# Performance work log

Measured on AMD Instinct MI355X. Metric: run time of the kernel, lower is better.

Reference implementation:

```python
import jax, jax.numpy as jnp
import numpy as np

ATT_TIMES = 2
EPS = 1e-12  # torch F.normalize eps

N_NODES = 200000
EMB_DIM = 256
ATT_NUM = 2


def setup_inputs() -> dict:
    key = jax.random.key(0)
    k1, k2 = jax.random.split(key)
    x = jax.random.normal(k1, (N_NODES, EMB_DIM), dtype=jnp.float32)
    # glorot/xavier-normal init for the att_num projection matrices W_i
    std = float(np.sqrt(2.0 / (EMB_DIM + EMB_DIM)))
    W = jax.random.normal(k2, (ATT_NUM, EMB_DIM, EMB_DIM), dtype=jnp.float32) * std
    return {"x": x, "W": W}


def _one_attention(x, Wi):
    """One attention head (att_style='dot', att_weight=True), iterated ATT_TIMES."""
    xi = x
    out = None
    for _ in range(ATT_TIMES):
        temp = jnp.mean(xi, axis=0, keepdims=True)          # (1, D)
        h_avg = jnp.tanh(temp @ Wi)                          # (1, D)
        # 'dot' style: interact with W = identity -> scores = x @ h_avg^T, (N, 1)
        scores = xi @ h_avg.T                                # (N, 1)
        # F.normalize(p=1, dim=1) on an (N,1) column: divide by max(|v|, eps)
        norm = jnp.maximum(jnp.sum(jnp.abs(scores), axis=1, keepdims=True), EPS)
        att = jax.nn.sigmoid(scores / norm)                  # (N, 1)
        out = att.T @ xi                                     # (1, D)
        xi = xi * att                                        # re-weight for next round
    return out


def reference(x, W):
    att_num = W.shape[0]
    outs = [_one_attention(x, W[i]) for i in range(att_num)]
    return jnp.concatenate(outs, axis=1)                     # (1, att_num * D)
```

## Files before the change

### kernel.cpp

```cpp
#include <hip/hip_runtime.h>
#include <math.h>

#define NROWS 200000
#define D 256
#define F4 64

#define NBLK 500
#define CHUNK 400
#define ITERS 25

#define WS_H1 0
#define WS_H2 512
#define WS_A  1024
#define WS_P1 401024
#define WS_P2 529024

__device__ __forceinline__ float att_sigmoid(float s) {
    float t = s / fmaxf(fabsf(s), 1e-12f);
    return 1.0f / (1.0f + __expf(-t));
}

__device__ __forceinline__ float wave_sum(float v) {
#pragma unroll
    for (int off = 1; off < 64; off <<= 1) v += __shfl_xor(v, off);
    return v;
}

__device__ __forceinline__ float dot4(float4 a, float4 b) {
    return fmaf(a.x, b.x, fmaf(a.y, b.y, fmaf(a.z, b.z, a.w * b.w)));
}

__global__ void __launch_bounds__(256) colsum_kernel(const float* __restrict__ x,
                                                     float* __restrict__ part) {
    const int tid = threadIdx.x, lane = tid & 63, wv = tid >> 6;
    const float4* x4 = reinterpret_cast<const float4*>(x);
    const size_t base = (size_t)(blockIdx.x * CHUNK + wv * 4) * F4 + lane;
    float4 cur[4], nxt[4];
#pragma unroll
    for (int j = 0; j < 4; ++j) cur[j] = x4[base + j * F4];
    float4 accA = make_float4(0.f, 0.f, 0.f, 0.f);
    float4 accB = make_float4(0.f, 0.f, 0.f, 0.f);
    for (int it = 0; it < ITERS; ++it) {
        if (it + 1 < ITERS) {
            size_t nb = base + (size_t)(it + 1) * 16 * F4;
#pragma unroll
            for (int j = 0; j < 4; ++j) nxt[j] = x4[nb + j * F4];
        }
        accA.x += cur[0].x + cur[1].x; accB.x += cur[2].x + cur[3].x;
        accA.y += cur[0].y + cur[1].y; accB.y += cur[2].y + cur[3].y;
        accA.z += cur[0].z + cur[1].z; accB.z += cur[2].z + cur[3].z;
        accA.w += cur[0].w + cur[1].w; accB.w += cur[2].w + cur[3].w;
        if (it + 1 < ITERS) {
#pragma unroll
            for (int j = 0; j < 4; ++j) cur[j] = nxt[j];
        }
    }
    accA.x += accB.x; accA.y += accB.y; accA.z += accB.z; accA.w += accB.w;
    __shared__ float4 sh[256];
    sh[tid] = accA;
    __syncthreads();
    if (tid < 64) {
        float4 a = sh[tid], b = sh[tid + 64], c = sh[tid + 128], d = sh[tid + 192];
        float4 s;
        s.x = (a.x + b.x) + (c.x + d.x);
        s.y = (a.y + b.y) + (c.y + d.y);
        s.z = (a.z + b.z) + (c.z + d.z);
        s.w = (a.w + b.w) + (c.w + d.w);
        reinterpret_cast<float4*>(part + blockIdx.x * 256)[tid] = s;
    }
}

__global__ void __launch_bounds__(256) hproj_fused(const float* __restrict__ W,
                                                   const float* __restrict__ part,
                                                   int width, int headColMul, float scale,
                                                   float* __restrict__ hout) {
    const int head = blockIdx.x;
    const int tid = threadIdx.x, lane = tid & 63, wv = tid >> 6;
    const float* p = part + head * headColMul + lane * 4;
    float4 s = make_float4(0.f, 0.f, 0.f, 0.f);
    for (int i = 0; i < 25; ++i) {
        float4 v[5];
#pragma unroll
        for (int k = 0; k < 5; ++k)
            v[k] = *reinterpret_cast<const float4*>(p + (size_t)(wv + (i * 5 + k) * 4) * width);
#pragma unroll
        for (int k = 0; k < 5; ++k) {
            s.x += v[k].x; s.y += v[k].y; s.z += v[k].z; s.w += v[k].w;
        }
    }
    __shared__ float4 red[4][64];
    __shared__ float vbuf[D];
    red[wv][lane] = s;
    __syncthreads();
    if (tid < 64) {
        float4 a = red[0][tid], b = red[1][tid], c = red[2][tid], d = red[3][tid];
        vbuf[tid * 4 + 0] = ((a.x + b.x) + (c.x + d.x)) * scale;
        vbuf[tid * 4 + 1] = ((a.y + b.y) + (c.y + d.y)) * scale;
        vbuf[tid * 4 + 2] = ((a.z + b.z) + (c.z + d.z)) * scale;
        vbuf[tid * 4 + 3] = ((a.w + b.w) + (c.w + d.w)) * scale;
    }
    __syncthreads();
    const float* Wh = W + head * D * D;
    float acc = 0.0f;
#pragma unroll 8
    for (int k = 0; k < D; ++k) acc = fmaf(vbuf[k], Wh[k * D + tid], acc);
    hout[head * D + tid] = tanhf(acc);
}

__global__ void __launch_bounds__(256) pass1_kernel(const float* __restrict__ x,
                                                    float* __restrict__ ws) {
    const float* h = ws + WS_H1;
    float* aA0 = ws + WS_A;
    float* aA1 = ws + WS_A + NROWS;
    float* part = ws + WS_P2;
    const int tid = threadIdx.x, lane = tid & 63, wv = tid >> 6;
    const int r0 = blockIdx.x * CHUNK + wv * 4;
    const float4* x4 = reinterpret_cast<const float4*>(x);
    const float4 h0v = reinterpret_cast<const float4*>(h)[lane];
    const float4 h1v = reinterpret_cast<const float4*>(h + D)[lane];
    float4 acc0 = make_float4(0.f, 0.f, 0.f, 0.f);
    float4 acc1 = make_float4(0.f, 0.f, 0.f, 0.f);
    const size_t base = (size_t)r0 * F4 + lane;
    float4 cur[4], nxt[4];
#pragma unroll
    for (int j = 0; j < 4; ++j) cur[j] = x4[base + j * F4];
    for (int it = 0; it < ITERS; ++it) {
        if (it + 1 < ITERS) {
            size_t nb = base + (size_t)(it + 1) * 16 * F4;
#pragma unroll
            for (int j = 0; j < 4; ++j) nxt[j] = x4[nb + j * F4];
        }
        float d0[4], d1[4];
#pragma unroll
        for (int j = 0; j < 4; ++j) { d0[j] = dot4(cur[j], h0v); d1[j] = dot4(cur[j], h1v); }
#pragma unroll
        for (int j = 0; j < 4; ++j) { d0[j] = wave_sum(d0[j]); d1[j] = wave_sum(d1[j]); }
        float a0[4], a1[4];
#pragma unroll
        for (int j = 0; j < 4; ++j) {
            a0[j] = att_sigmoid(d0[j]);
            a1[j] = att_sigmoid(d1[j]);
            acc0.x = fmaf(a0[j], cur[j].x, acc0.x);
            acc0.y = fmaf(a0[j], cur[j].y, acc0.y);
            acc0.z = fmaf(a0[j], cur[j].z, acc0.z);
            acc0.w = fmaf(a0[j], cur[j].w, acc0.w);
            acc1.x = fmaf(a1[j], cur[j].x, acc1.x);
            acc1.y = fmaf(a1[j], cur[j].y, acc1.y);
            acc1.z = fmaf(a1[j], cur[j].z, acc1.z);
            acc1.w = fmaf(a1[j], cur[j].w, acc1.w);
        }
        const int rb = r0 + it * 16;
        if (lane == 0)
            *reinterpret_cast<float4*>(aA0 + rb) = make_float4(a0[0], a0[1], a0[2], a0[3]);
        else if (lane == 1)
            *reinterpret_cast<float4*>(aA1 + rb) = make_float4(a1[0], a1[1], a1[2], a1[3]);
        if (it + 1 < ITERS) {
#pragma unroll
            for (int j = 0; j < 4; ++j) cur[j] = nxt[j];
        }
    }
    __shared__ float4 sh[2][256];
    sh[0][tid] = acc0;
    sh[1][tid] = acc1;
    __syncthreads();
    if (tid < 128) {
        int hh = tid >> 6;
        int t = tid & 63;
        float4 a = sh[hh][t], b = sh[hh][t + 64], c = sh[hh][t + 128], d = sh[hh][t + 192];
        float4 s;
        s.x = (a.x + b.x) + (c.x + d.x);
        s.y = (a.y + b.y) + (c.y + d.y);
        s.z = (a.z + b.z) + (c.z + d.z);
        s.w = (a.w + b.w) + (c.w + d.w);
        reinterpret_cast<float4*>(part + blockIdx.x * 512)[tid] = s;
    }
}

__global__ void __launch_bounds__(256) pass2_kernel(const float* __restrict__ x,
                                                    float* __restrict__ ws) {
    const float* h = ws + WS_H2;
    const float* aA0 = ws + WS_A;
    const float* aA1 = ws + WS_A + NROWS;
    float* part = ws + WS_P2;
    const int tid = threadIdx.x, lane = tid & 63, wv = tid >> 6;
    const int r0 = blockIdx.x * CHUNK + wv * 4;
    const float4* x4 = reinterpret_cast<const float4*>(x);
    const float4 h0v = reinterpret_cast<const float4*>(h)[lane];
    const float4 h1v = reinterpret_cast<const float4*>(h + D)[lane];
    float4 acc0 = make_float4(0.f, 0.f, 0.f, 0.f);
    float4 acc1 = make_float4(0.f, 0.f, 0.f, 0.f);
    const size_t base = (size_t)r0 * F4 + lane;
    float4 cur[4], nxt[4];
    float4 caa0, caa1, naa0, naa1;
#pragma unroll
    for (int j = 0; j < 4; ++j) cur[j] = x4[base + j * F4];
    caa0 = *reinterpret_cast<const float4*>(aA0 + r0);
    caa1 = *reinterpret_cast<const float4*>(aA1 + r0);
    for (int it = 0; it < ITERS; ++it) {
        if (it + 1 < ITERS) {
            size_t nb = base + (size_t)(it + 1) * 16 * F4;
#pragma unroll
            for (int j = 0; j < 4; ++j) nxt[j] = x4[nb + j * F4];
            naa0 = *reinterpret_cast<const float4*>(aA0 + r0 + (it + 1) * 16);
            naa1 = *reinterpret_cast<const float4*>(aA1 + r0 + (it + 1) * 16);
        }
        float d0[4], d1[4];
#pragma unroll
        for (int j = 0; j < 4; ++j) { d0[j] = dot4(cur[j], h0v); d1[j] = dot4(cur[j], h1v); }
#pragma unroll
        for (int j = 0; j < 4; ++j) { d0[j] = wave_sum(d0[j]); d1[j] = wave_sum(d1[j]); }
        float w0[4], w1[4];
        w0[0] = att_sigmoid(caa0.x * d0[0]) * caa0.x;
        w0[1] = att_sigmoid(caa0.y * d0[1]) * caa0.y;
        w0[2] = att_sigmoid(caa0.z * d0[2]) * caa0.z;
        w0[3] = att_sigmoid(caa0.w * d0[3]) * caa0.w;
        w1[0] = att_sigmoid(caa1.x * d1[0]) * caa1.x;
        w1[1] = att_sigmoid(caa1.y * d1[1]) * caa1.y;
        w1[2] = att_sigmoid(caa1.z * d1[2]) * caa1.z;
        w1[3] = att_sigmoid(caa1.w * d1[3]) * caa1.w;
#pragma unroll
        for (int j = 0; j < 4; ++j) {
            acc0.x = fmaf(w0[j], cur[j].x, acc0.x);
            acc0.y = fmaf(w0[j], cur[j].y, acc0.y);
            acc0.z = fmaf(w0[j], cur[j].z, acc0.z);
            acc0.w = fmaf(w0[j], cur[j].w, acc0.w);
            acc1.x = fmaf(w1[j], cur[j].x, acc1.x);
            acc1.y = fmaf(w1[j], cur[j].y, acc1.y);
            acc1.z = fmaf(w1[j], cur[j].z, acc1.z);
            acc1.w = fmaf(w1[j], cur[j].w, acc1.w);
        }
        if (it + 1 < ITERS) {
#pragma unroll
            for (int j = 0; j < 4; ++j) cur[j] = nxt[j];
            caa0 = naa0; caa1 = naa1;
        }
    }
    __shared__ float4 sh[2][256];
    sh[0][tid] = acc0;
    sh[1][tid] = acc1;
    __syncthreads();
    if (tid < 128) {
        int hh = tid >> 6;
        int t = tid & 63;
        float4 a = sh[hh][t], b = sh[hh][t + 64], c = sh[hh][t + 128], d = sh[hh][t + 192];
        float4 s;
        s.x = (a.x + b.x) + (c.x + d.x);
        s.y = (a.y + b.y) + (c.y + d.y);
        s.z = (a.z + b.z) + (c.z + d.z);
        s.w = (a.w + b.w) + (c.w + d.w);
        reinterpret_cast<float4*>(part + blockIdx.x * 512)[tid] = s;
    }
}

__global__ void __launch_bounds__(256) out_reduce(const float* __restrict__ part,
                                                  float* __restrict__ out) {
    const int head = blockIdx.x;
    const int tid = threadIdx.x, lane = tid & 63, wv = tid >> 6;
    const float* p = part + head * 256 + lane * 4;
    float4 s = make_float4(0.f, 0.f, 0.f, 0.f);
    for (int i = 0; i < 25; ++i) {
        float4 v[5];
#pragma unroll
        for (int k = 0; k < 5; ++k)
            v[k] = *reinterpret_cast<const float4*>(p + (size_t)(wv + (i * 5 + k) * 4) * 512);
#pragma unroll
        for (int k = 0; k < 5; ++k) {
            s.x += v[k].x; s.y += v[k].y; s.z += v[k].z; s.w += v[k].w;
        }
    }
    __shared__ float4 red[4][64];
    red[wv][lane] = s;
    __syncthreads();
    if (tid < 64) {
        float4 a = red[0][tid], b = red[1][tid], c = red[2][tid], d = red[3][tid];
        float4 o;
        o.x = (a.x + b.x) + (c.x + d.x);
        o.y = (a.y + b.y) + (c.y + d.y);
        o.z = (a.z + b.z) + (c.z + d.z);
        o.w = (a.w + b.w) + (c.w + d.w);
        reinterpret_cast<float4*>(out + head * 256)[tid] = o;
    }
}

extern "C" void kernel_launch(void* const* d_in, const int* in_sizes, int n_in,
                              void* d_out, int out_size, void* d_ws, size_t ws_size,
                              hipStream_t stream) {
    const float* x = (const float*)d_in[0];
    const float* W = (const float*)d_in[1];
    float* out = (float*)d_out;
    float* ws = (float*)d_ws;

    colsum_kernel<<<dim3(NBLK), dim3(256), 0, stream>>>(x, ws + WS_P1);
    hproj_fused<<<dim3(2), dim3(256), 0, stream>>>(W, ws + WS_P1, 256, 0, 1.0f / NROWS, ws + WS_H1);
    pass1_kernel<<<dim3(NBLK), dim3(256), 0, stream>>>(x, ws);
    hproj_fused<<<dim3(2), dim3(256), 0, stream>>>(W, ws + WS_P2, 512, 256, 1.0f / NROWS, ws + WS_H2);
    pass2_kernel<<<dim3(NBLK), dim3(256), 0, stream>>>(x, ws);
    out_reduce<<<dim3(2), dim3(256), 0, stream>>>(ws + WS_P2, out);
}
```

Before: 167.2 us.

## Map one row per 16-lane group and raise block count for streaming passes

```diff
diff --git a/kernel.cpp b/kernel.cpp
--- a/kernel.cpp
+++ b/kernel.cpp
@@ -5,29 +5,29 @@
 #define D 256
 #define F4 64
 
-#define NBLK 500
-#define CHUNK 400
-#define ITERS 25
+#define NBLK 1250
+#define CHUNK 160
+#define ITERS 10
 
 #define WS_H1 0
 #define WS_H2 512
 #define WS_A  1024
 #define WS_P1 401024
-#define WS_P2 529024
+#define WS_P2 721024
 
 __device__ __forceinline__ float att_sigmoid(float s) {
     float t = s / fmaxf(fabsf(s), 1e-12f);
     return 1.0f / (1.0f + __expf(-t));
 }
 
-__device__ __forceinline__ float wave_sum(float v) {
-#pragma unroll
-    for (int off = 1; off < 64; off <<= 1) v += __shfl_xor(v, off);
-    return v;
-}
-
 __device__ __forceinline__ float dot4(float4 a, float4 b) {
     return fmaf(a.x, b.x, fmaf(a.y, b.y, fmaf(a.z, b.z, a.w * b.w)));
+}
+
+__device__ __forceinline__ float group16_sum(float v) {
+#pragma unroll
+    for (int off = 1; off < 16; off <<= 1) v += __shfl_xor(v, off);
+    return v;
 }
 
 __global__ void __launch_bounds__(256) colsum_kernel(const float* __restrict__ x,
@@ -66,27 +66,22 @@
         s.y = (a.y + b.y) + (c.y + d.y);
         s.z = (a.z + b.z) + (c.z + d.z);
         s.w = (a.w + b.w) + (c.w + d.w);
-        reinterpret_cast<float4*>(part + blockIdx.x * 256)[tid] = s;
+        reinterpret_cast<float4*>(part)[blockIdx.x * 64 + tid] = s;
     }
 }
 
 __global__ void __launch_bounds__(256) hproj_fused(const float* __restrict__ W,
                                                    const float* __restrict__ part,
-                                                   int width, int headColMul, float scale,
+                                                   int width4, int headOff4, float scale,
                                                    float* __restrict__ hout) {
     const int head = blockIdx.x;
     const int tid = threadIdx.x, lane = tid & 63, wv = tid >> 6;
-    const float* p = part + head * headColMul + lane * 4;
+    const float4* p4 = reinterpret_cast<const float4*>(part) + head * headOff4 + lane;
     float4 s = make_float4(0.f, 0.f, 0.f, 0.f);
-    for (int i = 0; i < 25; ++i) {
-        float4 v[5];
-#pragma unroll
-        for (int k = 0; k < 5; ++k)
-            v[k] = *reinterpret_cast<const float4*>(p + (size_t)(wv + (i * 5 + k) * 4) * width);
-#pragma unroll
-        for (int k = 0; k < 5; ++k) {
-            s.x += v[k].x; s.y += v[k].y; s.z += v[k].z; s.w += v[k].w;
-        }
+#pragma unroll 5
+    for (int r = wv; r < NBLK; r += 4) {
+        float4 v = p4[(size_t)r * width4];
+        s.x += v.x; s.y += v.y; s.z += v.z; s.w += v.w;
     }
     __shared__ float4 red[4][64];
     __shared__ float vbuf[D];
@@ -114,65 +109,70 @@
     float* aA1 = ws + WS_A + NROWS;
     float* part = ws + WS_P2;
     const int tid = threadIdx.x, lane = tid & 63, wv = tid >> 6;
-    const int r0 = blockIdx.x * CHUNK + wv * 4;
+    const int sub = lane >> 4, li = lane & 15;
     const float4* x4 = reinterpret_cast<const float4*>(x);
-    const float4 h0v = reinterpret_cast<const float4*>(h)[lane];
-    const float4 h1v = reinterpret_cast<const float4*>(h + D)[lane];
-    float4 acc0 = make_float4(0.f, 0.f, 0.f, 0.f);
-    float4 acc1 = make_float4(0.f, 0.f, 0.f, 0.f);
-    const size_t base = (size_t)r0 * F4 + lane;
+    const float4* h4 = reinterpret_cast<const float4*>(h);
+    float4 h0v[4], h1v[4];
+#pragma unroll
+    for (int t = 0; t < 4; ++t) { h0v[t] = h4[li + 16 * t]; h1v[t] = h4[64 + li + 16 * t]; }
+    const int row0 = blockIdx.x * CHUNK + wv * 4 + sub;
+    const size_t base = (size_t)row0 * F4 + li;
     float4 cur[4], nxt[4];
 #pragma unroll
-    for (int j = 0; j < 4; ++j) cur[j] = x4[base + j * F4];
+    for (int t = 0; t < 4; ++t) cur[t] = x4[base + 16 * t];
+    float4 acc0[4], acc1[4];
+#pragma unroll
+    for (int t = 0; t < 4; ++t) {
+        acc0[t] = make_float4(0.f, 0.f, 0.f, 0.f);
+        acc1[t] = make_float4(0.f, 0.f, 0.f, 0.f);
+    }
     for (int it = 0; it < ITERS; ++it) {
         if (it + 1 < ITERS) {
             size_t nb = base + (size_t)(it + 1) * 16 * F4;
 #pragma unroll
-            for (int j = 0; j < 4; ++j) nxt[j] = x4[nb + j * F4];
-        }
-        float d0[4], d1[4];
-#pragma unroll
-        for (int j = 0; j < 4; ++j) { d0[j] = dot4(cur[j], h0v); d1[j] = dot4(cur[j], h1v); }
-#pragma unroll
-        for (int j = 0; j < 4; ++j) { d0[j] = wave_sum(d0[j]); d1[j] = wave_sum(d1[j]); }
-        float a0[4], a1[4];
-#pragma unroll
-        for (int j = 0; j < 4; ++j) {
-            a0[j] = att_sigmoid(d0[j]);
-            a1[j] = att_sigmoid(d1[j]);
-            acc0.x = fmaf(a0[j], cur[j].x, acc0.x);
-            acc0.y = fmaf(a0[j], cur[j].y, acc0.y);
-            acc0.z = fmaf(a0[j], cur[j].z, acc0.z);
-            acc0.w = fmaf(a0[j], cur[j].w, acc0.w);
-            acc1.x = fmaf(a1[j], cur[j].x, acc1.x);
-            acc1.y = fmaf(a1[j], cur[j].y, acc1.y);
-            acc1.z = fmaf(a1[j], cur[j].z, acc1.z);
-            acc1.w = fmaf(a1[j], cur[j].w, acc1.w);
-        }
-        const int rb = r0 + it * 16;
-        if (lane == 0)
-            *reinterpret_cast<float4*>(aA0 + rb) = make_float4(a0[0], a0[1], a0[2], a0[3]);
-        else if (lane == 1)
-            *reinterpret_cast<float4*>(aA1 + rb) = make_float4(a1[0], a1[1], a1[2], a1[3]);
-        if (it + 1 < ITERS) {
-#pragma unroll
-            for (int j = 0; j < 4; ++j) cur[j] = nxt[j];
-        }
-    }
-    __shared__ float4 sh[2][256];
-    sh[0][tid] = acc0;
-    sh[1][tid] = acc1;
+            for (int t = 0; t < 4; ++t) nxt[t] = x4[nb + 16 * t];
+        }
+        float d0 = (dot4(cur[0], h0v[0]) + dot4(cur[1], h0v[1]))
+                 + (dot4(cur[2], h0v[2]) + dot4(cur[3], h0v[3]));
+        float d1 = (dot4(cur[0], h1v[0]) + dot4(cur[1], h1v[1]))
+                 + (dot4(cur[2], h1v[2]) + dot4(cur[3], h1v[3]));
+        d0 = group16_sum(d0);
+        d1 = group16_sum(d1);
+        float a0 = att_sigmoid(d0);
+        float a1 = att_sigmoid(d1);
+        if (li == 0) {
+            aA0[row0 + it * 16] = a0;
+            aA1[row0 + it * 16] = a1;
+        }
+#pragma unroll
+        for (int t = 0; t < 4; ++t) {
+            acc0[t].x = fmaf(a0, cur[t].x, acc0[t].x);
+            acc0[t].y = fmaf(a0, cur[t].y, acc0[t].y);
+            acc0[t].z = fmaf(a0, cur[t].z, acc0[t].z);
+            acc0[t].w = fmaf(a0, cur[t].w, acc0[t].w);
+            acc1[t].x = fmaf(a1, cur[t].x, acc1[t].x);
+            acc1[t].y = fmaf(a1, cur[t].y, acc1[t].y);
+            acc1[t].z = fmaf(a1, cur[t].z, acc1[t].z);
+            acc1[t].w = fmaf(a1, cur[t].w, acc1[t].w);
+        }
+        if (it + 1 < ITERS) {
+#pragma unroll
+            for (int t = 0; t < 4; ++t) cur[t] = nxt[t];
+        }
+    }
+    __shared__ float4 sh[256][9];
+#pragma unroll
+    for (int t = 0; t < 4; ++t) { sh[tid][t] = acc0[t]; sh[tid][4 + t] = acc1[t]; }
     __syncthreads();
     if (tid < 128) {
-        int hh = tid >> 6;
-        int t = tid & 63;
-        float4 a = sh[hh][t], b = sh[hh][t + 64], c = sh[hh][t + 128], d = sh[hh][t + 192];
-        float4 s;
-        s.x = (a.x + b.x) + (c.x + d.x);
-        s.y = (a.y + b.y) + (c.y + d.y);
-        s.z = (a.z + b.z) + (c.z + d.z);
-        s.w = (a.w + b.w) + (c.w + d.w);
-        reinterpret_cast<float4*>(part + blockIdx.x * 512)[tid] = s;
+        const int hh = tid >> 6, f = tid & 63, fl = f & 15, ft = f >> 4;
+        float4 s = make_float4(0.f, 0.f, 0.f, 0.f);
+#pragma unroll
+        for (int g = 0; g < 16; ++g) {
+            float4 v = sh[(g >> 2) * 64 + (g & 3) * 16 + fl][hh * 4 + ft];
+            s.x += v.x; s.y += v.y; s.z += v.z; s.w += v.w;
+        }
+        reinterpret_cast<float4*>(part)[blockIdx.x * 128 + tid] = s;
     }
 }
 
@@ -183,72 +183,72 @@
     const float* aA1 = ws + WS_A + NROWS;
     float* part = ws + WS_P2;
     const int tid = threadIdx.x, lane = tid & 63, wv = tid >> 6;
-    const int r0 = blockIdx.x * CHUNK + wv * 4;
+    const int sub = lane >> 4, li = lane & 15;
     const float4* x4 = reinterpret_cast<const float4*>(x);
-    const float4 h0v = reinterpret_cast<const float4*>(h)[lane];
-    const float4 h1v = reinterpret_cast<const float4*>(h + D)[lane];
-    float4 acc0 = make_float4(0.f, 0.f, 0.f, 0.f);
-    float4 acc1 = make_float4(0.f, 0.f, 0.f, 0.f);
-    const size_t base = (size_t)r0 * F4 + lane;
+    const float4* h4 = reinterpret_cast<const float4*>(h);
+    float4 h0v[4], h1v[4];
+#pragma unroll
+    for (int t = 0; t < 4; ++t) { h0v[t] = h4[li + 16 * t]; h1v[t] = h4[64 + li + 16 * t]; }
+    const int row0 = blockIdx.x * CHUNK + wv * 4 + sub;
+    const size_t base = (size_t)row0 * F4 + li;
     float4 cur[4], nxt[4];
-    float4 caa0, caa1, naa0, naa1;
-#pragma unroll
-    for (int j = 0; j < 4; ++j) cur[j] = x4[base + j * F4];
-    caa0 = *reinterpret_cast<const float4*>(aA0 + r0);
-    caa1 = *reinterpret_cast<const float4*>(aA1 + r0);
+    float caa0, caa1, naa0, naa1;
+#pragma unroll
+    for (int t = 0; t < 4; ++t) cur[t] = x4[base + 16 * t];
+    caa0 = aA0[row0];
+    caa1 = aA1[row0];
+    float4 acc0[4], acc1[4];
+#pragma unroll
+    for (int t = 0; t < 4; ++t) {
+        acc0[t] = make_float4(0.f, 0.f, 0.f, 0.f);
+        acc1[t] = make_float4(0.f, 0.f, 0.f, 0.f);
+    }
     for (int it = 0; it < ITERS; ++it) {
         if (it + 1 < ITERS) {
             size_t nb = base + (size_t)(it + 1) * 16 * F4;
 #pragma unroll
-            for (int j = 0; j < 4; ++j) nxt[j] = x4[nb + j * F4];
-            naa0 = *reinterpret_cast<const float4*>(aA0 + r0 + (it + 1) * 16);
-            naa1 = *reinterpret_cast<const float4*>(aA1 + r0 + (it + 1) * 16);
-        }
-        float d0[4], d1[4];
-#pragma unroll
-        for (int j = 0; j < 4; ++j) { d0[j] = dot4(cur[j], h0v); d1[j] = dot4(cur[j], h1v); }
-#pragma unroll
-        for (int j = 0; j < 4; ++j) { d0[j] = wave_sum(d0[j]); d1[j] = wave_sum(d1[j]); }
-        float w0[4], w1[4];
-        w0[0] = att_sigmoid(caa0.x * d0[0]) * caa0.x;
-        w0[1] = att_sigmoid(caa0.y * d0[1]) * caa0.y;
-        w0[2] = att_sigmoid(caa0.z * d0[2]) * caa0.z;
-        w0[3] = att_sigmoid(caa0.w * d0[3]) * caa0.w;
-        w1[0] = att_sigmoid(caa1.x * d1[0]) * caa1.x;
-        w1[1] = att_sigmoid(caa1.y * d1[1]) * caa1.y;
-        w1[2] = att_sigmoid(caa1.z * d1[2]) * caa1.z;
-        w1[3] = att_sigmoid(caa1.w * d1[3]) * caa1.w;
-#pragma unroll
-        for (int j = 0; j < 4; ++j) {
-            acc0.x = fmaf(w0[j], cur[j].x, acc0.x);
-            acc0.y = fmaf(w0[j], cur[j].y, acc0.y);
-            acc0.z = fmaf(w0[j], cur[j].z, acc0.z);
-            acc0.w = fmaf(w0[j], cur[j].w, acc0.w);
-            acc1.x = fmaf(w1[j], cur[j].x, acc1.x);
-            acc1.y = fmaf(w1[j], cur[j].y, acc1.y);
-            acc1.z = fmaf(w1[j], cur[j].z, acc1.z);
-            acc1.w = fmaf(w1[j], cur[j].w, acc1.w);
-        }
-        if (it + 1 < ITERS) {
-#pragma unroll
-            for (int j = 0; j < 4; ++j) cur[j] = nxt[j];
+            for (int t = 0; t < 4; ++t) nxt[t] = x4[nb + 16 * t];
+            naa0 = aA0[row0 + (it + 1) * 16];
+            naa1 = aA1[row0 + (it + 1) * 16];
+        }
+        float d0 = (dot4(cur[0], h0v[0]) + dot4(cur[1], h0v[1]))
+                 + (dot4(cur[2], h0v[2]) + dot4(cur[3], h0v[3]));
+        float d1 = (dot4(cur[0], h1v[0]) + dot4(cur[1], h1v[1]))
+                 + (dot4(cur[2], h1v[2]) + dot4(cur[3], h1v[3]));
+        d0 = group16_sum(d0);
+        d1 = group16_sum(d1);
+        float w0 = att_sigmoid(caa0 * d0) * caa0;
+        float w1 = att_sigmoid(caa1 * d1) * caa1;
+#pragma unroll
+        for (int t = 0; t < 4; ++t) {
+            acc0[t].x = fmaf(w0, cur[t].x, acc0[t].x);
+            acc0[t].y = fmaf(w0, cur[t].y, acc0[t].y);
+            acc0[t].z = fmaf(w0, cur[t].z, acc0[t].z);
+            acc0[t].w = fmaf(w0, cur[t].w, acc0[t].w);
+            acc1[t].x = fmaf(w1, cur[t].x, acc1[t].x);
+            acc1[t].y = fmaf(w1, cur[t].y, acc1[t].y);
+            acc1[t].z = fmaf(w1, cur[t].z, acc1[t].z);
+            acc1[t].w = fmaf(w1, cur[t].w, acc1[t].w);
+        }
+        if (it + 1 < ITERS) {
+#pragma unroll
+            for (int t = 0; t < 4; ++t) cur[t] = nxt[t];
             caa0 = naa0; caa1 = naa1;
         }
     }
-    __shared__ float4 sh[2][256];
-    sh[0][tid] = acc0;
-    sh[1][tid] = acc1;
+    __shared__ float4 sh[256][9];
+#pragma unroll
+    for (int t = 0; t < 4; ++t) { sh[tid][t] = acc0[t]; sh[tid][4 + t] = acc1[t]; }
     __syncthreads();
     if (tid < 128) {
-        int hh = tid >> 6;
-        int t = tid & 63;
-        float4 a = sh[hh][t], b = sh[hh][t + 64], c = sh[hh][t + 128], d = sh[hh][t + 192];
-        float4 s;
-        s.x = (a.x + b.x) + (c.x + d.x);
-        s.y = (a.y + b.y) + (c.y + d.y);
-        s.z = (a.z + b.z) + (c.z + d.z);
-        s.w = (a.w + b.w) + (c.w + d.w);
-        reinterpret_cast<float4*>(part + blockIdx.x * 512)[tid] = s;
+        const int hh = tid >> 6, f = tid & 63, fl = f & 15, ft = f >> 4;
+        float4 s = make_float4(0.f, 0.f, 0.f, 0.f);
+#pragma unroll
+        for (int g = 0; g < 16; ++g) {
+            float4 v = sh[(g >> 2) * 64 + (g & 3) * 16 + fl][hh * 4 + ft];
+            s.x += v.x; s.y += v.y; s.z += v.z; s.w += v.w;
+        }
+        reinterpret_cast<float4*>(part)[blockIdx.x * 128 + tid] = s;
     }
 }
 
@@ -256,17 +256,12 @@
                                                   float* __restrict__ out) {
     const int head = blockIdx.x;
     const int tid = threadIdx.x, lane = tid & 63, wv = tid >> 6;
-    const float* p = part + head * 256 + lane * 4;
+    const float4* p4 = reinterpret_cast<const float4*>(part) + head * 64 + lane;
     float4 s = make_float4(0.f, 0.f, 0.f, 0.f);
-    for (int i = 0; i < 25; ++i) {
-        float4 v[5];
-#pragma unroll
-        for (int k = 0; k < 5; ++k)
-            v[k] = *reinterpret_cast<const float4*>(p + (size_t)(wv + (i * 5 + k) * 4) * 512);
-#pragma unroll
-        for (int k = 0; k < 5; ++k) {
-            s.x += v[k].x; s.y += v[k].y; s.z += v[k].z; s.w += v[k].w;
-        }
+#pragma unroll 5
+    for (int r = wv; r < NBLK; r += 4) {
+        float4 v = p4[(size_t)r * 128];
+        s.x += v.x; s.y += v.y; s.z += v.z; s.w += v.w;
     }
     __shared__ float4 red[4][64];
     red[wv][lane] = s;
@@ -278,7 +273,7 @@
         o.y = (a.y + b.y) + (c.y + d.y);
         o.z = (a.z + b.z) + (c.z + d.z);
         o.w = (a.w + b.w) + (c.w + d.w);
-        reinterpret_cast<float4*>(out + head * 256)[tid] = o;
+        reinterpret_cast<float4*>(out)[head * 64 + tid] = o;
     }
 }
 
@@ -291,9 +286,9 @@
     float* ws = (float*)d_ws;
 
     colsum_kernel<<<dim3(NBLK), dim3(256), 0, stream>>>(x, ws + WS_P1);
-    hproj_fused<<<dim3(2), dim3(256), 0, stream>>>(W, ws + WS_P1, 256, 0, 1.0f / NROWS, ws + WS_H1);
+    hproj_fused<<<dim3(2), dim3(256), 0, stream>>>(W, ws + WS_P1, 64, 0, 1.0f / NROWS, ws + WS_H1);
     pass1_kernel<<<dim3(NBLK), dim3(256), 0, stream>>>(x, ws);
-    hproj_fused<<<dim3(2), dim3(256), 0, stream>>>(W, ws + WS_P2, 512, 256, 1.0f / NROWS, ws + WS_H2);
+    hproj_fused<<<dim3(2), dim3(256), 0, stream>>>(W, ws + WS_P2, 128, 64, 1.0f / NROWS, ws + WS_H2);
     pass2_kernel<<<dim3(NBLK), dim3(256), 0, stream>>>(x, ws);
     out_reduce<<<dim3(2), dim3(256), 0, stream>>>(ws + WS_P2, out);
 }
```

After: 184.3 us. 10.2% more time.

## Fuse six kernel launches into one cooperative kernel with grid syncs

Applied to the files above, without the earlier changes.

```diff
diff --git a/kernel.cpp b/kernel.cpp
--- a/kernel.cpp
+++ b/kernel.cpp
@@ -1,5 +1,8 @@
 #include <hip/hip_runtime.h>
+#include <hip/hip_cooperative_groups.h>
 #include <math.h>
+
+namespace cg = cooperative_groups;
 
 #define NROWS 200000
 #define D 256
@@ -30,11 +33,33 @@
     return fmaf(a.x, b.x, fmaf(a.y, b.y, fmaf(a.z, b.z, a.w * b.w)));
 }
 
-__global__ void __launch_bounds__(256) colsum_kernel(const float* __restrict__ x,
-                                                     float* __restrict__ part) {
+__device__ __forceinline__ void acc4(float4& acc, float s, const float4& v) {
+    acc.x = fmaf(s, v.x, acc.x);
+    acc.y = fmaf(s, v.y, acc.y);
+    acc.z = fmaf(s, v.z, acc.z);
+    acc.w = fmaf(s, v.w, acc.w);
+}
+
+__device__ __forceinline__ float4 add4(float4 a, float4 b, float4 c, float4 d) {
+    float4 s;
+    s.x = (a.x + b.x) + (c.x + d.x);
+    s.y = (a.y + b.y) + (c.y + d.y);
+    s.z = (a.z + b.z) + (c.z + d.z);
+    s.w = (a.w + b.w) + (c.w + d.w);
+    return s;
+}
+
+struct Smem {
+    float4 sh[2][256];
+    float vbuf[D];
+};
+
+
+__device__ void colsum_body(const float* __restrict__ x, float* __restrict__ part,
+                            int blk, Smem& sm) {
     const int tid = threadIdx.x, lane = tid & 63, wv = tid >> 6;
     const float4* x4 = reinterpret_cast<const float4*>(x);
-    const size_t base = (size_t)(blockIdx.x * CHUNK + wv * 4) * F4 + lane;
+    const size_t base = (size_t)(blk * CHUNK + wv * 4) * F4 + lane;
     float4 cur[4], nxt[4];
 #pragma unroll
     for (int j = 0; j < 4; ++j) cur[j] = x4[base + j * F4];
@@ -56,65 +81,53 @@
         }
     }
     accA.x += accB.x; accA.y += accB.y; accA.z += accB.z; accA.w += accB.w;
-    __shared__ float4 sh[256];
-    sh[tid] = accA;
+    sm.sh[0][tid] = accA;
     __syncthreads();
     if (tid < 64) {
-        float4 a = sh[tid], b = sh[tid + 64], c = sh[tid + 128], d = sh[tid + 192];
-        float4 s;
-        s.x = (a.x + b.x) + (c.x + d.x);
-        s.y = (a.y + b.y) + (c.y + d.y);
-        s.z = (a.z + b.z) + (c.z + d.z);
-        s.w = (a.w + b.w) + (c.w + d.w);
-        reinterpret_cast<float4*>(part + blockIdx.x * 256)[tid] = s;
-    }
-}
-
-__global__ void __launch_bounds__(256) hproj_fused(const float* __restrict__ W,
-                                                   const float* __restrict__ part,
-                                                   int width, int headColMul, float scale,
-                                                   float* __restrict__ hout) {
-    const int head = blockIdx.x;
-    const int tid = threadIdx.x, lane = tid & 63, wv = tid >> 6;
-    const float* p = part + head * headColMul + lane * 4;
+        float4 s = add4(sm.sh[0][tid], sm.sh[0][tid + 64], sm.sh[0][tid + 128], sm.sh[0][tid + 192]);
+        reinterpret_cast<float4*>(part)[blk * 64 + tid] = s;
+    }
+    __syncthreads();
+}
+
+__device__ void hproj_body(const float* __restrict__ W, const float* __restrict__ part,
+                           int width4, int headOff4, float scale,
+                           float* __restrict__ hout, int head, Smem& sm) {
+    const int tid = threadIdx.x, lane = tid & 63, wv = tid >> 6;
+    const float4* p4 = reinterpret_cast<const float4*>(part) + head * headOff4 + lane;
     float4 s = make_float4(0.f, 0.f, 0.f, 0.f);
-    for (int i = 0; i < 25; ++i) {
-        float4 v[5];
-#pragma unroll
-        for (int k = 0; k < 5; ++k)
-            v[k] = *reinterpret_cast<const float4*>(p + (size_t)(wv + (i * 5 + k) * 4) * width);
-#pragma unroll
-        for (int k = 0; k < 5; ++k) {
-            s.x += v[k].x; s.y += v[k].y; s.z += v[k].z; s.w += v[k].w;
-        }
-    }
-    __shared__ float4 red[4][64];
-    __shared__ float vbuf[D];
-    red[wv][lane] = s;
+#pragma unroll 5
+    for (int r = wv; r < NBLK; r += 4) {
+        float4 v = p4[(size_t)r * width4];
+        s.x += v.x; s.y += v.y; s.z += v.z; s.w += v.w;
+    }
+    float4* red = &sm.sh[0][0];
+    red[wv * 64 + lane] = s;
     __syncthreads();
     if (tid < 64) {
-        float4 a = red[0][tid], b = red[1][tid], c = red[2][tid], d = red[3][tid];
-        vbuf[tid * 4 + 0] = ((a.x + b.x) + (c.x + d.x)) * scale;
-        vbuf[tid * 4 + 1] = ((a.y + b.y) + (c.y + d.y)) * scale;
-        vbuf[tid * 4 + 2] = ((a.z + b.z) + (c.z + d.z)) * scale;
-        vbuf[tid * 4 + 3] = ((a.w + b.w) + (c.w + d.w)) * scale;
+        float4 v = add4(red[tid], red[64 + tid], red[128 + tid], red[192 + tid]);
+        sm.vbuf[tid * 4 + 0] = v.x * scale;
+        sm.vbuf[tid * 4 + 1] = v.y * scale;
+        sm.vbuf[tid * 4 + 2] = v.z * scale;
+        sm.vbuf[tid * 4 + 3] = v.w * scale;
     }
     __syncthreads();
     const float* Wh = W + head * D * D;
     float acc = 0.0f;
 #pragma unroll 8
-    for (int k = 0; k < D; ++k) acc = fmaf(vbuf[k], Wh[k * D + tid], acc);
+    for (int k = 0; k < D; ++k) acc = fmaf(sm.vbuf[k], Wh[k * D + tid], acc);
     hout[head * D + tid] = tanhf(acc);
-}
-
-__global__ void __launch_bounds__(256) pass1_kernel(const float* __restrict__ x,
-                                                    float* __restrict__ ws) {
+    __syncthreads();
+}
+
+__device__ void pass1_body(const float* __restrict__ x, float* __restrict__ ws,
+                           int blk, Smem& sm) {
     const float* h = ws + WS_H1;
     float* aA0 = ws + WS_A;
     float* aA1 = ws + WS_A + NROWS;
     float* part = ws + WS_P2;
     const int tid = threadIdx.x, lane = tid & 63, wv = tid >> 6;
-    const int r0 = blockIdx.x * CHUNK + wv * 4;
+    const int r0 = blk * CHUNK + wv * 4;
     const float4* x4 = reinterpret_cast<const float4*>(x);
     const float4 h0v = reinterpret_cast<const float4*>(h)[lane];
     const float4 h1v = reinterpret_cast<const float4*>(h + D)[lane];
@@ -140,14 +153,8 @@
         for (int j = 0; j < 4; ++j) {
             a0[j] = att_sigmoid(d0[j]);
             a1[j] = att_sigmoid(d1[j]);
-            acc0.x = fmaf(a0[j], cur[j].x, acc0.x);
-            acc0.y = fmaf(a0[j], cur[j].y, acc0.y);
-            acc0.z = fmaf(a0[j], cur[j].z, acc0.z);
-            acc0.w = fmaf(a0[j], cur[j].w, acc0.w);
-            acc1.x = fmaf(a1[j], cur[j].x, acc1.x);
-            acc1.y = fmaf(a1[j], cur[j].y, acc1.y);
-            acc1.z = fmaf(a1[j], cur[j].z, acc1.z);
-            acc1.w = fmaf(a1[j], cur[j].w, acc1.w);
+            acc4(acc0, a0[j], cur[j]);
+            acc4(acc1, a1[j], cur[j]);
         }
         const int rb = r0 + it * 16;
         if (lane == 0)
@@ -159,31 +166,27 @@
             for (int j = 0; j < 4; ++j) cur[j] = nxt[j];
         }
     }
-    __shared__ float4 sh[2][256];
-    sh[0][tid] = acc0;
-    sh[1][tid] = acc1;
+    sm.sh[0][tid] = acc0;
+    sm.sh[1][tid] = acc1;
     __syncthreads();
     if (tid < 128) {
         int hh = tid >> 6;
         int t = tid & 63;
-        float4 a = sh[hh][t], b = sh[hh][t + 64], c = sh[hh][t + 128], d = sh[hh][t + 192];
-        float4 s;
-        s.x = (a.x + b.x) + (c.x + d.x);
-        s.y = (a.y + b.y) + (c.y + d.y);
-        s.z = (a.z + b.z) + (c.z + d.z);
-        s.w = (a.w + b.w) + (c.w + d.w);
-        reinterpret_cast<float4*>(part + blockIdx.x * 512)[tid] = s;
-    }
-}
-
-__global__ void __launch_bounds__(256) pass2_kernel(const float* __restrict__ x,
-                                                    float* __restrict__ ws) {
+        const float4* s = &sm.sh[hh][0];
+        float4 v = add4(s[t], s[t + 64], s[t + 128], s[t + 192]);
+        reinterpret_cast<float4*>(part)[blk * 128 + tid] = v;
+    }
+    __syncthreads();
+}
+
+__device__ void pass2_body(const float* __restrict__ x, float* __restrict__ ws,
+                           int blk, Smem& sm) {
     const float* h = ws + WS_H2;
     const float* aA0 = ws + WS_A;
     const float* aA1 = ws + WS_A + NROWS;
     float* part = ws + WS_P2;
     const int tid = threadIdx.x, lane = tid & 63, wv = tid >> 6;
-    const int r0 = blockIdx.x * CHUNK + wv * 4;
+    const int r0 = blk * CHUNK + wv * 4;
     const float4* x4 = reinterpret_cast<const float4*>(x);
     const float4 h0v = reinterpret_cast<const float4*>(h)[lane];
     const float4 h1v = reinterpret_cast<const float4*>(h + D)[lane];
@@ -220,14 +223,8 @@
         w1[3] = att_sigmoid(caa1.w * d1[3]) * caa1.w;
 #pragma unroll
         for (int j = 0; j < 4; ++j) {
-            acc0.x = fmaf(w0[j], cur[j].x, acc0.x);
-            acc0.y = fmaf(w0[j], cur[j].y, acc0.y);
-            acc0.z = fmaf(w0[j], cur[j].z, acc0.z);
-            acc0.w = fmaf(w0[j], cur[j].w, acc0.w);
-            acc1.x = fmaf(w1[j], cur[j].x, acc1.x);
-            acc1.y = fmaf(w1[j], cur[j].y, acc1.y);
-            acc1.z = fmaf(w1[j], cur[j].z, acc1.z);
-            acc1.w = fmaf(w1[j], cur[j].w, acc1.w);
+            acc4(acc0, w0[j], cur[j]);
+            acc4(acc1, w1[j], cur[j]);
         }
         if (it + 1 < ITERS) {
 #pragma unroll
@@ -235,51 +232,57 @@
             caa0 = naa0; caa1 = naa1;
         }
     }
-    __shared__ float4 sh[2][256];
-    sh[0][tid] = acc0;
-    sh[1][tid] = acc1;
+    sm.sh[0][tid] = acc0;
+    sm.sh[1][tid] = acc1;
     __syncthreads();
     if (tid < 128) {
         int hh = tid >> 6;
         int t = tid & 63;
-        float4 a = sh[hh][t], b = sh[hh][t + 64], c = sh[hh][t + 128], d = sh[hh][t + 192];
-        float4 s;
-        s.x = (a.x + b.x) + (c.x + d.x);
-        s.y = (a.y + b.y) + (c.y + d.y);
-        s.z = (a.z + b.z) + (c.z + d.z);
-        s.w = (a.w + b.w) + (c.w + d.w);
-        reinterpret_cast<float4*>(part + blockIdx.x * 512)[tid] = s;
-    }
-}
-
-__global__ void __launch_bounds__(256) out_reduce(const float* __restrict__ part,
-                                                  float* __restrict__ out) {
-    const int head = blockIdx.x;
-    const int tid = threadIdx.x, lane = tid & 63, wv = tid >> 6;
-    const float* p = part + head * 256 + lane * 4;
+        const float4* s = &sm.sh[hh][0];
+        float4 v = add4(s[t], s[t + 64], s[t + 128], s[t + 192]);
+        reinterpret_cast<float4*>(part)[blk * 128 + tid] = v;
+    }
+    __syncthreads();
+}
+
+__device__ void out_reduce_body(const float* __restrict__ part, float* __restrict__ out,
+                                int head, Smem& sm) {
+    const int tid = threadIdx.x, lane = tid & 63, wv = tid >> 6;
+    const float4* p4 = reinterpret_cast<const float4*>(part) + head * 64 + lane;
     float4 s = make_float4(0.f, 0.f, 0.f, 0.f);
-    for (int i = 0; i < 25; ++i) {
-        float4 v[5];
-#pragma unroll
-        for (int k = 0; k < 5; ++k)
-            v[k] = *reinterpret_cast<const float4*>(p + (size_t)(wv + (i * 5 + k) * 4) * 512);
-#pragma unroll
-        for (int k = 0; k < 5; ++k) {
-            s.x += v[k].x; s.y += v[k].y; s.z += v[k].z; s.w += v[k].w;
-        }
-    }
-    __shared__ float4 red[4][64];
-    red[wv][lane] = s;
+#pragma unroll 5
+    for (int r = wv; r < NBLK; r += 4) {
+        float4 v = p4[(size_t)r * 128];
+        s.x += v.x; s.y += v.y; s.z += v.z; s.w += v.w;
+    }
+    float4* red = &sm.sh[0][0];
+    red[wv * 64 + lane] = s;
     __syncthreads();
     if (tid < 64) {
-        float4 a = red[0][tid], b = red[1][tid], c = red[2][tid], d = red[3][tid];
-        float4 o;
-        o.x = (a.x + b.x) + (c.x + d.x);
-        o.y = (a.y + b.y) + (c.y + d.y);
-        o.z = (a.z + b.z) + (c.z + d.z);
-        o.w = (a.w + b.w) + (c.w + d.w);
-        reinterpret_cast<float4*>(out + head * 256)[tid] = o;
-    }
+        float4 o = add4(red[tid], red[64 + tid], red[128 + tid], red[192 + tid]);
+        reinterpret_cast<float4*>(out)[head * 64 + tid] = o;
+    }
+}
+
+__global__ void __launch_bounds__(256, 2) fused_kernel(const float* __restrict__ x,
+                                                       const float* __restrict__ W,
+                                                       float* __restrict__ out,
+                                                       float* __restrict__ ws) {
+    cg::grid_group grid = cg::this_grid();
+    __shared__ Smem sm;
+    const int b = blockIdx.x;
+
+    colsum_body(x, ws + WS_P1, b, sm);
+    grid.sync();
+    if (b < 2) hproj_body(W, ws + WS_P1, 64, 0, 1.0f / NROWS, ws + WS_H1, b, sm);
+    grid.sync();
+    pass1_body(x, ws, b, sm);
+    grid.sync();
+    if (b < 2) hproj_body(W, ws + WS_P2, 128, 64, 1.0f / NROWS, ws + WS_H2, b, sm);
+    grid.sync();
+    pass2_body(x, ws, b, sm);
+    grid.sync();
+    if (b < 2) out_reduce_body(ws + WS_P2, out, b, sm);
 }
 
 extern "C" void kernel_launch(void* const* d_in, const int* in_sizes, int n_in,
@@ -290,10 +293,7 @@
     float* out = (float*)d_out;
     float* ws = (float*)d_ws;
 
-    colsum_kernel<<<dim3(NBLK), dim3(256), 0, stream>>>(x, ws + WS_P1);
-    hproj_fused<<<dim3(2), dim3(256), 0, stream>>>(W, ws + WS_P1, 256, 0, 1.0f / NROWS, ws + WS_H1);
-    pass1_kernel<<<dim3(NBLK), dim3(256), 0, stream>>>(x, ws);
-    hproj_fused<<<dim3(2), dim3(256), 0, stream>>>(W, ws + WS_P2, 512, 256, 1.0f / NROWS, ws + WS_H2);
-    pass2_kernel<<<dim3(NBLK), dim3(256), 0, stream>>>(x, ws);
-    out_reduce<<<dim3(2), dim3(256), 0, stream>>>(ws + WS_P2, out);
-}
+    void* args[] = {(void*)&x, (void*)&W, (void*)&out, (void*)&ws};
+    hipLaunchCooperativeKernel((void*)fused_kernel, dim3(NBLK), dim3(256),
+                               args, 0, stream);
+}
```

After: 426.1 us. 155% more time.
